# Optimization experiments

Hardware: AMD Instinct MI355X
Metric: run time of the kernel (lower is better)

Reference implementation:

```python
import jax, jax.numpy as jnp
import numpy as np

# Fingertip landmark indices (end_ldmrk = [12,24,36,48,57] in flat coords -> landmarks {4,8,12,16,19})
_END_LANDMARKS = {4, 8, 12, 16, 19}

def _build_pairs():
    pairs = []
    for j in range(20):  # index in range(0, 60, 3) -> landmark j = index//3
        start = j + 1 if j in _END_LANDMARKS else j + 2  # skip adjacent landmark unless fingertip
        for k in range(start, 21):  # x in range(start, 63, 3) -> landmark k = x//3
            pairs.append((j, k))
    return np.asarray(pairs, dtype=np.int32)  # [195, 2]

_PAIRS = _build_pairs()
_I = jnp.asarray(_PAIRS[:, 0])  # [195]
_J = jnp.asarray(_PAIRS[:, 1])  # [195]


def setup_inputs() -> dict:
    key = jax.random.key(0)
    B = 1_000_000
    return {"tensor": jax.random.normal(key, (B, 63), dtype=jnp.float32)}


def reference(tensor):
    # tensor: [B, 63] = 21 landmarks x (x, y, z); distances use only x, y.
    B = tensor.shape[0]
    xy = tensor.reshape(B, 21, 3)[..., :2]          # [B, 21, 2]
    d = xy[:, _I, :] - xy[:, _J, :]                 # [B, 195, 2] only needed pairs
    feats = jnp.sqrt(jnp.sum(d * d, axis=-1))       # [B, 195] 2D Euclidean distances
    return jnp.concatenate([tensor, feats], axis=-1)  # [B, 258]
```

## Files before the change

### kernel.cpp

```cpp
#include <hip/hip_runtime.h>
#include <math.h>

#define ROWS 16
#define NPAIRS 195
#define NTHREADS 256
#define ROW_OUT 258
#define NLM 21
#define TILE_F (ROWS * ROW_OUT)
#define GRID 1024

typedef float f32x4 __attribute__((ext_vector_type(4)));

struct CodeTab { unsigned int c[NPAIRS]; };

constexpr CodeTab make_codes() {
    CodeTab t{};
    int n = 0;
    for (int a = 0; a < 20; ++a) {
        bool tip = (a == 4) || (a == 8) || (a == 12) || (a == 16) || (a == 19);
        int start = tip ? a + 1 : a + 2;
        for (int b = start; b < 21; ++b) {
            t.c[n] = (unsigned int)a | ((unsigned int)b << 16);
            ++n;
        }
    }
    return t;
}

__constant__ CodeTab CODES = make_codes();

__device__ __forceinline__ void scatter_tile(float* __restrict__ tile,
                                             float2* __restrict__ xy2,
                                             const f32x4 v, int t) {
    const int f = t * 4;
#pragma unroll
    for (int e = 0; e < 4; ++e) {
        const int g = f + e;
        const int row = g / 63;
        const int col = g - row * 63;
        tile[row * ROW_OUT + col] = v[e];
        const int lm = col / 3;
        const int c3 = col - lm * 3;
        if (c3 == 0) xy2[row * NLM + lm].x = v[e];
        else if (c3 == 1) xy2[row * NLM + lm].y = v[e];
    }
}

__device__ __forceinline__ void compute_dists(float* __restrict__ tile,
                                              const float2* __restrict__ xy2,
                                              int t) {
#pragma unroll
    for (int k = 0; k < 13; ++k) {
        const int idx = t + k * NTHREADS;
        if (idx < ROWS * NPAIRS) {
            const int row = idx / NPAIRS;
            const int p = idx - row * NPAIRS;
            const unsigned int c = CODES.c[p];
            const float2 a = xy2[row * NLM + (int)(c & 0xffu)];
            const float2 b = xy2[row * NLM + (int)(c >> 16)];
            const float dx = a.x - b.x;
            const float dy = a.y - b.y;
            tile[row * ROW_OUT + 63 + p] = sqrtf(dx * dx + dy * dy);
        }
    }
}

__global__ __launch_bounds__(NTHREADS)
void HandKineticLayer_18545668784560_kernel(const float* __restrict__ in,
                                            float* __restrict__ out,
                                            int B) {
    __shared__ __align__(16) float tile[2][TILE_F];
    __shared__ float2 xy2[2][ROWS * NLM];

    const int t = threadIdx.x;
    const int ntiles = B / ROWS;

    const int tile0 = blockIdx.x;
    if (tile0 < ntiles) {
        if (t < 252) {
            const f32x4* __restrict__ in4 =
                reinterpret_cast<const f32x4*>(in + (size_t)tile0 * (ROWS * 63));
            const f32x4 v = __builtin_nontemporal_load(&in4[t]);
            scatter_tile(tile[0], xy2[0], v, t);
        }
        __syncthreads();
    }

    int i = 0;
    for (int tl = tile0; tl < ntiles; tl += GRID, ++i) {
        const int cur = i & 1;
        const int nxt = tl + GRID;
        f32x4 vn{};
        const bool have_next = (nxt < ntiles) && (t < 252);
        if (have_next) {
            const f32x4* __restrict__ in4 =
                reinterpret_cast<const f32x4*>(in + (size_t)nxt * (ROWS * 63));
            vn = __builtin_nontemporal_load(&in4[t]);
        }

        compute_dists(tile[cur], xy2[cur], t);
        __syncthreads();

        {
            const f32x4* __restrict__ tl4 =
                reinterpret_cast<const f32x4*>(&tile[cur][0]);
            f32x4* __restrict__ o4 =
                reinterpret_cast<f32x4*>(out + (size_t)tl * TILE_F);
#pragma unroll
            for (int k = t; k < TILE_F / 4; k += NTHREADS) {
                __builtin_nontemporal_store(tl4[k], &o4[k]);
            }
        }

        if (have_next) {
            scatter_tile(tile[cur ^ 1], xy2[cur ^ 1], vn, t);
        }
        __syncthreads();
    }

    const int rem = B - ntiles * ROWS;
    if (rem > 0 && blockIdx.x == (unsigned)(ntiles % GRID)) {
        const int rowBase = ntiles * ROWS;
        const int nelem = rem * 63;
        for (int g = t; g < nelem; g += NTHREADS) {
            const float val = in[(size_t)rowBase * 63 + g];
            const int row = g / 63;
            const int col = g - row * 63;
            tile[0][row * ROW_OUT + col] = val;
            const int lm = col / 3;
            const int c3 = col - lm * 3;
            if (c3 == 0) xy2[0][row * NLM + lm].x = val;
            else if (c3 == 1) xy2[0][row * NLM + lm].y = val;
        }
        __syncthreads();
        const int total = rem * NPAIRS;
        for (int idx = t; idx < total; idx += NTHREADS) {
            const int row = idx / NPAIRS;
            const int p = idx - row * NPAIRS;
            const unsigned int c = CODES.c[p];
            const float2 a = xy2[0][row * NLM + (int)(c & 0xffu)];
            const float2 b = xy2[0][row * NLM + (int)(c >> 16)];
            const float dx = a.x - b.x;
            const float dy = a.y - b.y;
            tile[0][row * ROW_OUT + 63 + p] = sqrtf(dx * dx + dy * dy);
        }
        __syncthreads();
        const int nout = rem * ROW_OUT;
        for (int k = t; k < nout; k += NTHREADS) {
            out[(size_t)rowBase * ROW_OUT + k] = tile[0][k];
        }
    }
}

extern "C" void kernel_launch(void* const* d_in, const int* in_sizes, int n_in,
                              void* d_out, int out_size, void* d_ws, size_t ws_size,
                              hipStream_t stream) {
    const float* in = (const float*)d_in[0];
    float* out = (float*)d_out;
    const int B = in_sizes[0] / 63;
    hipLaunchKernelGGL(HandKineticLayer_18545668784560_kernel,
                       dim3(GRID), dim3(NTHREADS), 0, stream,
                       in, out, B);
}
```

Before: 272.2 us.

## Restructure distance computation per row with paired steps and lighter LDS barriers

Distance work is re-mapped so 16 threads own one row and each handles two pairs per step, using a packed step table. A 'fast' flag shares the left landmark when two consecutive pairs have the same i and adjacent j. The landmark buffer is padded to 24 entries per row. Input scatter gets a fast path when all four values fall in one row. `__syncthreads` is replaced by a raw lgkmcnt-wait plus barrier, sqrt uses the AMDGPU builtin, and launch bounds request 4 blocks per CU. The duplicated last pair writes one element past each row's distance block, so an extra fix-up pass and barrier restore column 0 of the next row. This adds a fragile cross-row dependency.

Result: slower. 306.2 us (+12.5%).

```diff
diff --git a/kernel.cpp b/kernel.cpp
--- a/kernel.cpp
+++ b/kernel.cpp
@@ -6,71 +6,116 @@
 #define NTHREADS 256
 #define ROW_OUT 258
 #define NLM 21
+#define XY_PAD 24
 #define TILE_F (ROWS * ROW_OUT)
+#define IN_F (ROWS * 63)
 #define GRID 1024
+#define NSTEPS 98
 
 typedef float f32x4 __attribute__((ext_vector_type(4)));
-
-struct CodeTab { unsigned int c[NPAIRS]; };
-
-constexpr CodeTab make_codes() {
-    CodeTab t{};
+typedef float f32x2 __attribute__((ext_vector_type(2)));
+
+#define LDS_BARRIER() asm volatile("s_waitcnt lgkmcnt(0)\n\ts_barrier" ::: "memory")
+
+struct StepTab { unsigned int m[NSTEPS]; };
+
+constexpr StepTab make_steps() {
+    int pi[NPAIRS] = {}; int pj[NPAIRS] = {};
     int n = 0;
     for (int a = 0; a < 20; ++a) {
-        bool tip = (a == 4) || (a == 8) || (a == 12) || (a == 16) || (a == 19);
-        int start = tip ? a + 1 : a + 2;
-        for (int b = start; b < 21; ++b) {
-            t.c[n] = (unsigned int)a | ((unsigned int)b << 16);
-            ++n;
-        }
+        bool tip = (a==4)||(a==8)||(a==12)||(a==16)||(a==19);
+        int start = tip ? a+1 : a+2;
+        for (int b = start; b < 21; ++b) { pi[n]=a; pj[n]=b; ++n; }
+    }
+    StepTab t{};
+    for (int s = 0; s < NSTEPS; ++s) {
+        int p0 = 2*s; int p1 = 2*s+1 < NPAIRS ? 2*s+1 : NPAIRS-1;
+        unsigned i0=pi[p0], j0=pj[p0], i1=pi[p1], j1=pj[p1];
+        unsigned fast = (i0==i1 && j1==j0+1) ? 1u : 0u;
+        t.m[s] = i0 | (j0<<5) | (i1<<10) | (j1<<15) | (fast<<20);
     }
     return t;
 }
 
-__constant__ CodeTab CODES = make_codes();
+__constant__ StepTab STEPS = make_steps();
 
 __device__ __forceinline__ void scatter_tile(float* __restrict__ tile,
                                              float2* __restrict__ xy2,
                                              const f32x4 v, int t) {
     const int f = t * 4;
+    const int row0 = f / 63;
+    const int col0 = f - row0 * 63;
+    if (col0 <= 59) {
+        float* __restrict__ p = tile + row0 * ROW_OUT + col0;
+        p[0]=v[0]; p[1]=v[1]; p[2]=v[2]; p[3]=v[3];
+        float2* __restrict__ xr = xy2 + row0 * XY_PAD;
 #pragma unroll
-    for (int e = 0; e < 4; ++e) {
-        const int g = f + e;
-        const int row = g / 63;
-        const int col = g - row * 63;
-        tile[row * ROW_OUT + col] = v[e];
-        const int lm = col / 3;
-        const int c3 = col - lm * 3;
-        if (c3 == 0) xy2[row * NLM + lm].x = v[e];
-        else if (c3 == 1) xy2[row * NLM + lm].y = v[e];
+        for (int e = 0; e < 4; ++e) {
+            const int col = col0 + e;
+            const int lm = col / 3;
+            const int c3 = col - lm * 3;
+            if (c3 == 0) xr[lm].x = v[e];
+            else if (c3 == 1) xr[lm].y = v[e];
+        }
+    } else {
+#pragma unroll
+        for (int e = 0; e < 4; ++e) {
+            const int g = f + e;
+            const int row = g / 63;
+            const int col = g - row * 63;
+            tile[row * ROW_OUT + col] = v[e];
+            const int lm = col / 3;
+            const int c3 = col - lm * 3;
+            if (c3 == 0) xy2[row * XY_PAD + lm].x = v[e];
+            else if (c3 == 1) xy2[row * XY_PAD + lm].y = v[e];
+        }
     }
 }
 
 __device__ __forceinline__ void compute_dists(float* __restrict__ tile,
                                               const float2* __restrict__ xy2,
                                               int t) {
+    const int r = t >> 4;
+    const int q = t & 15;
+    float* __restrict__ drow = tile + r * ROW_OUT + 63;
+    const float2* __restrict__ xr = xy2 + r * XY_PAD;
+    for (int s = q; s < NSTEPS; s += 16) {
+        const unsigned m = STEPS.m[s];
+        const int i0 = (int)(m & 31u);
+        const int j0 = (int)((m >> 5) & 31u);
+        const int j1 = (int)((m >> 15) & 31u);
+        float2 a0, a1, b0, b1;
+        if (m & (1u << 20)) {
+            b0 = xr[j0]; b1 = xr[j0 + 1];
+            a0 = xr[i0]; a1 = a0;
+        } else {
+            a0 = xr[i0]; a1 = xr[i0 + 1];
+            b0 = xr[j0]; b1 = xr[j1];
+        }
+        const float dx0 = a0.x - b0.x, dy0 = a0.y - b0.y;
+        const float dx1 = a1.x - b1.x, dy1 = a1.y - b1.y;
+        const float d0 = __builtin_amdgcn_sqrtf(dx0*dx0 + dy0*dy0);
+        const float d1 = __builtin_amdgcn_sqrtf(dx1*dx1 + dy1*dy1);
+        drow[2*s]     = d0;
+        drow[2*s + 1] = d1;
+    }
+}
+
+__device__ __forceinline__ void store_tile(const float* __restrict__ tile,
+                                           float* __restrict__ outp, int t) {
 #pragma unroll
-    for (int k = 0; k < 13; ++k) {
-        const int idx = t + k * NTHREADS;
-        if (idx < ROWS * NPAIRS) {
-            const int row = idx / NPAIRS;
-            const int p = idx - row * NPAIRS;
-            const unsigned int c = CODES.c[p];
-            const float2 a = xy2[row * NLM + (int)(c & 0xffu)];
-            const float2 b = xy2[row * NLM + (int)(c >> 16)];
-            const float dx = a.x - b.x;
-            const float dy = a.y - b.y;
-            tile[row * ROW_OUT + 63 + p] = sqrtf(dx * dx + dy * dy);
-        }
-    }
-}
-
-__global__ __launch_bounds__(NTHREADS)
+    for (int k = t; k < TILE_F / 4; k += NTHREADS) {
+        const f32x4 o = *(const f32x4*)(tile + 4 * k);
+        __builtin_nontemporal_store(o, (f32x4*)(outp + 4 * k));
+    }
+}
+
+__global__ __launch_bounds__(NTHREADS, 4)
 void HandKineticLayer_18545668784560_kernel(const float* __restrict__ in,
                                             float* __restrict__ out,
                                             int B) {
-    __shared__ __align__(16) float tile[2][TILE_F];
-    __shared__ float2 xy2[2][ROWS * NLM];
+    __shared__ __align__(16) float tile[2][TILE_F + 8];
+    __shared__ float2 xy2[2][ROWS * XY_PAD];
 
     const int t = threadIdx.x;
     const int ntiles = B / ROWS;
@@ -79,11 +124,11 @@
     if (tile0 < ntiles) {
         if (t < 252) {
             const f32x4* __restrict__ in4 =
-                reinterpret_cast<const f32x4*>(in + (size_t)tile0 * (ROWS * 63));
+                reinterpret_cast<const f32x4*>(in + (size_t)tile0 * IN_F);
             const f32x4 v = __builtin_nontemporal_load(&in4[t]);
             scatter_tile(tile[0], xy2[0], v, t);
         }
-        __syncthreads();
+        LDS_BARRIER();
     }
 
     int i = 0;
@@ -94,28 +139,24 @@
         const bool have_next = (nxt < ntiles) && (t < 252);
         if (have_next) {
             const f32x4* __restrict__ in4 =
-                reinterpret_cast<const f32x4*>(in + (size_t)nxt * (ROWS * 63));
+                reinterpret_cast<const f32x4*>(in + (size_t)nxt * IN_F);
             vn = __builtin_nontemporal_load(&in4[t]);
         }
 
         compute_dists(tile[cur], xy2[cur], t);
-        __syncthreads();
-
-        {
-            const f32x4* __restrict__ tl4 =
-                reinterpret_cast<const f32x4*>(&tile[cur][0]);
-            f32x4* __restrict__ o4 =
-                reinterpret_cast<f32x4*>(out + (size_t)tl * TILE_F);
-#pragma unroll
-            for (int k = t; k < TILE_F / 4; k += NTHREADS) {
-                __builtin_nontemporal_store(tl4[k], &o4[k]);
-            }
-        }
+        LDS_BARRIER();
+        if ((t & 15) == 1 && (t >> 4) >= 1) {
+            const int r = t >> 4;
+            tile[cur][r * ROW_OUT + 0] = xy2[cur][r * XY_PAD + 0].x;
+        }
+        LDS_BARRIER();
+
+        store_tile(tile[cur], out + (size_t)tl * TILE_F, t);
 
         if (have_next) {
             scatter_tile(tile[cur ^ 1], xy2[cur ^ 1], vn, t);
         }
-        __syncthreads();
+        LDS_BARRIER();
     }
 
     const int rem = B - ntiles * ROWS;
@@ -129,20 +170,21 @@
             tile[0][row * ROW_OUT + col] = val;
             const int lm = col / 3;
             const int c3 = col - lm * 3;
-            if (c3 == 0) xy2[0][row * NLM + lm].x = val;
-            else if (c3 == 1) xy2[0][row * NLM + lm].y = val;
+            if (c3 == 0) xy2[0][row * XY_PAD + lm].x = val;
+            else if (c3 == 1) xy2[0][row * XY_PAD + lm].y = val;
         }
         __syncthreads();
         const int total = rem * NPAIRS;
         for (int idx = t; idx < total; idx += NTHREADS) {
             const int row = idx / NPAIRS;
             const int p = idx - row * NPAIRS;
-            const unsigned int c = CODES.c[p];
-            const float2 a = xy2[0][row * NLM + (int)(c & 0xffu)];
-            const float2 b = xy2[0][row * NLM + (int)(c >> 16)];
-            const float dx = a.x - b.x;
-            const float dy = a.y - b.y;
-            tile[0][row * ROW_OUT + 63 + p] = sqrtf(dx * dx + dy * dy);
+            const unsigned m = STEPS.m[p >> 1];
+            const int ii = (p & 1) ? (int)((m>>10)&31u) : (int)(m & 31u);
+            const int jj = (p & 1) ? (int)((m>>15)&31u) : (int)((m>>5)&31u);
+            const float2 a = xy2[0][row * XY_PAD + ii];
+            const float2 b = xy2[0][row * XY_PAD + jj];
+            const float dx = a.x - b.x, dy = a.y - b.y;
+            tile[0][row * ROW_OUT + 63 + p] = __builtin_amdgcn_sqrtf(dx*dx + dy*dy);
         }
         __syncthreads();
         const int nout = rem * ROW_OUT;
```
